# Kernel optimization log

Measured on AMD Instinct MI355X. Metric: run time of the kernel, lower is better.

Reference implementation:

```python
import jax, jax.numpy as jnp
import numpy as np

D_MODEL = 1024
NUM_HEADS = 16
D_HEAD = D_MODEL // NUM_HEADS
ROPE_THETA = 10000.0


def _rope(x, pos):
    # x: [..., S, d_head]; rotate consecutive pairs (2i, 2i+1)
    half = x.shape[-1] // 2
    inv_freq = ROPE_THETA ** (-jnp.arange(half, dtype=jnp.float32) * 2.0 / x.shape[-1])
    ang = pos[:, None].astype(jnp.float32) * inv_freq[None, :]  # [S, half]
    cos, sin = jnp.cos(ang), jnp.sin(ang)
    x1, x2 = x[..., 0::2], x[..., 1::2]
    r1 = x1 * cos - x2 * sin
    r2 = x1 * sin + x2 * cos
    return jnp.stack([r1, r2], axis=-1).reshape(x.shape)


def setup_inputs() -> dict:
    key = jax.random.key(0)
    ks = jax.random.split(key, 5)
    s = 1.0 / np.sqrt(D_MODEL)
    return {
        "q_weight": jax.random.normal(ks[0], (D_MODEL, D_MODEL), jnp.float32) * s,
        "k_weight": jax.random.normal(ks[1], (D_MODEL, D_MODEL), jnp.float32) * s,
        "v_weight": jax.random.normal(ks[2], (D_MODEL, D_MODEL), jnp.float32) * s,
        "o_weight": jax.random.normal(ks[3], (D_MODEL, D_MODEL), jnp.float32) * s,
        "in_features": jax.random.normal(ks[4], (2, 2048, D_MODEL), jnp.float32),
    }


def reference(q_weight, k_weight, v_weight, o_weight, in_features):
    S = in_features.shape[-2]
    qw = q_weight.reshape(NUM_HEADS, D_HEAD, D_MODEL)
    kw = k_weight.reshape(NUM_HEADS, D_HEAD, D_MODEL)
    vw = v_weight.reshape(NUM_HEADS, D_HEAD, D_MODEL)
    # [B, H, S, d_head]
    q = jnp.einsum('bsj,nhj->bnsh', in_features, qw)
    k = jnp.einsum('bsj,nhj->bnsh', in_features, kw)
    v = jnp.einsum('bsj,nhj->bnsh', in_features, vw)
    pos = jnp.arange(S)
    q = _rope(q, pos)
    k = _rope(k, pos)
    scale = 1.0 / jnp.sqrt(jnp.asarray(D_HEAD, dtype=q.dtype))
    scores = jnp.einsum('bnqh,bnkh->bnqk', q, k) * scale  # [B,H,S,S]
    causal = jnp.tril(jnp.ones((S, S), dtype=bool))
    scores = jnp.where(causal, scores, jnp.asarray(-jnp.inf, dtype=scores.dtype))
    attn = jax.nn.softmax(scores, axis=-1)
    out = jnp.einsum('bnqk,bnkh->bnqh', attn, v)  # [B,H,S,d_head]
    out = jnp.swapaxes(out, -2, -3).reshape(*out.shape[:-3], S, D_MODEL)
    return jnp.einsum('ji,bki->bkj', o_weight, out)
```

## Files before the change

### kernel.cpp

```cpp
#include <hip/hip_runtime.h>
#include <math.h>

typedef __attribute__((ext_vector_type(8))) short bf16x8;
typedef __attribute__((ext_vector_type(4))) short bf16x4;
typedef __attribute__((ext_vector_type(4))) float f32x4;
typedef __attribute__((ext_vector_type(2))) unsigned int u32x2;

static constexpr int D_MODEL = 1024;
static constexpr int SEQ = 2048;
static constexpr int BATCH = 2;
static constexpr int M_TOT = BATCH * SEQ;

__device__ __forceinline__ unsigned short f2bf(float f) {
  unsigned int u = __builtin_bit_cast(unsigned int, f);
  u += 0x7fffu + ((u >> 16) & 1u);
  return (unsigned short)(u >> 16);
}

__device__ __forceinline__ float bf2f(unsigned short u) {
  return __builtin_bit_cast(float, (unsigned int)u << 16);
}

__device__ __forceinline__ unsigned int cvtpk(float lo, float hi) {
  unsigned int r;
  asm volatile("v_cvt_pk_bf16_f32 %0, %1, %2" : "=v"(r) : "v"(lo), "v"(hi));
  return r;
}

__device__ __forceinline__ void gld16(const unsigned short* g, unsigned short* l) {
  __builtin_amdgcn_global_load_lds(
      (const __attribute__((address_space(1))) unsigned int*)g,
      (__attribute__((address_space(3))) unsigned int*)l, 16, 0, 0);
}

__global__ void prep_all(const float* __restrict__ x,
                         const float* __restrict__ qw, const float* __restrict__ kw,
                         const float* __restrict__ vw, const float* __restrict__ ow,
                         unsigned short* __restrict__ Xb,
                         unsigned short* __restrict__ Wqb,
                         float2* __restrict__ ct2) {
  constexpr int NX = M_TOT * D_MODEL / 4;
  constexpr int NW = D_MODEL * D_MODEL;
  const int i = blockIdx.x * blockDim.x + threadIdx.x;
  if (i < NX) {
    const float4 v = reinterpret_cast<const float4*>(x)[i];
    ushort4 o;
    o.x = f2bf(v.x); o.y = f2bf(v.y); o.z = f2bf(v.z); o.w = f2bf(v.w);
    reinterpret_cast<ushort4*>(Xb)[i] = o;
  } else if (i < NX + NW) {
    const int k = i - NX;
    const int which = k >> 18;
    const int off = k & 262143;
    const float* src = (which == 0) ? qw : (which == 1) ? kw : (which == 2) ? vw : ow;
    const float4 v = reinterpret_cast<const float4*>(src)[off];
    ushort4 o;
    o.x = f2bf(v.x); o.y = f2bf(v.y); o.z = f2bf(v.z); o.w = f2bf(v.w);
    reinterpret_cast<ushort4*>(Wqb)[k] = o;
  } else {
    const int k = i - NX - NW;
    const int s = k >> 5;
    const int p = k & 31;
    const float inv_freq = powf(10000.0f, -(float)p / 32.0f);
    const float ang = (float)s * inv_freq;
    const int psw = p ^ (((s >> 2) & 1) << 3);
    float2 cs; cs.x = cosf(ang); cs.y = sinf(ang);
    ct2[s * 32 + psw] = cs;
  }
}

template <int BM, int BN, int MODE>
__global__ __launch_bounds__(256, 2)
void gemm2(const unsigned short* __restrict__ A,
           const unsigned short* __restrict__ W,
           unsigned short* __restrict__ Qd,
           unsigned short* __restrict__ Kd,
           unsigned short* __restrict__ Vd,
           float* __restrict__ Fd,
           const float2* __restrict__ ct2) {
  constexpr int MI = BM / 32, NI = BN / 32;
  constexpr int NKT = D_MODEL / 64;
  constexpr int LOADS = BM / 32 + BN / 32;
  __shared__ __align__(16) unsigned short smem[2 * (BM + BN) * 64];
  unsigned short* Asm = smem;
  unsigned short* Bsm = smem + 2 * BM * 64;
  const int tid  = threadIdx.x;
  const int lane = tid & 63;
  const int wave = tid >> 6;
  const int wm = wave >> 1, wn = wave & 1;
  const int m0 = blockIdx.y * BM;
  const int n0 = blockIdx.x * BN;
  const int lr = lane & 15, lg = lane >> 4;

  auto stage = [&](int buf, int kt) {
    const int k0 = kt * 64;
#pragma unroll
    for (int c = 0; c < BM / 32; ++c) {
      const int ch = c * 4 + wave;
      const int row = ch * 8 + (lane >> 3);
      gld16(&A[(size_t)(m0 + row) * D_MODEL + k0 + ((lane & 7) ^ (row & 7)) * 8],
            &Asm[buf * BM * 64 + ch * 512]);
    }
#pragma unroll
    for (int c = 0; c < BN / 32; ++c) {
      const int ch = c * 4 + wave;
      const int row = ch * 8 + (lane >> 3);
      gld16(&W[(size_t)(n0 + row) * D_MODEL + k0 + ((lane & 7) ^ (row & 7)) * 8],
            &Bsm[buf * BN * 64 + ch * 512]);
    }
  };

  f32x4 acc[MI][NI] = {};

  stage(0, 0);
  stage(1, 1);
  __builtin_amdgcn_sched_barrier(0);

  for (int kt = 0; kt < NKT; ++kt) {
    const int cur = kt & 1;
    if (kt + 1 < NKT) {
      if constexpr (LOADS == 8) asm volatile("s_waitcnt vmcnt(8)" ::: "memory");
      else                      asm volatile("s_waitcnt vmcnt(6)" ::: "memory");
    } else {
      asm volatile("s_waitcnt vmcnt(0)" ::: "memory");
    }
    __builtin_amdgcn_s_barrier();
    __builtin_amdgcn_sched_barrier(0);

    bf16x8 af[MI][2], bfr[NI][2];
#pragma unroll
    for (int i = 0; i < MI; ++i)
#pragma unroll
      for (int ks = 0; ks < 2; ++ks) {
        const int R = wm * (BM / 2) + i * 16 + lr;
        const int p = (ks * 4 + lg) ^ (R & 7);
        af[i][ks] = *reinterpret_cast<const bf16x8*>(&Asm[cur * BM * 64 + R * 64 + p * 8]);
      }
#pragma unroll
    for (int j = 0; j < NI; ++j)
#pragma unroll
      for (int ks = 0; ks < 2; ++ks) {
        const int R = wn * (BN / 2) + j * 16 + lr;
        const int p = (ks * 4 + lg) ^ (R & 7);
        bfr[j][ks] = *reinterpret_cast<const bf16x8*>(&Bsm[cur * BN * 64 + R * 64 + p * 8]);
      }
    asm volatile("s_waitcnt lgkmcnt(0)" ::: "memory");
    __builtin_amdgcn_sched_barrier(0);
    __builtin_amdgcn_s_barrier();
    __builtin_amdgcn_sched_barrier(0);

    if (kt + 2 < NKT) stage(cur, kt + 2);
    __builtin_amdgcn_sched_barrier(0);

#pragma unroll
    for (int ks = 0; ks < 2; ++ks)
#pragma unroll
      for (int i = 0; i < MI; ++i)
#pragma unroll
        for (int j = 0; j < NI; ++j)
          acc[i][j] = __builtin_amdgcn_mfma_f32_16x16x32_bf16(af[i][ks], bfr[j][ks], acc[i][j], 0, 0, 0);
  }

  if constexpr (MODE == 2) {
#pragma unroll
    for (int i = 0; i < MI; ++i)
#pragma unroll
      for (int j = 0; j < NI; ++j)
#pragma unroll
        for (int r = 0; r < 4; ++r) {
          const int gm = m0 + wm * (BM / 2) + i * 16 + lg * 4 + r;
          const int gc = n0 + wn * (BN / 2) + j * 16 + lr;
          Fd[(size_t)gm * D_MODEL + gc] = acc[i][j][r];
        }
  } else {
    const int t = n0 >> 10;
    const int b = m0 >> 11;
    const int s_base = m0 & 2047;
    if (t < 2) {
      unsigned short* dstQ = (t == 0) ? Qd : Kd;
      const unsigned short* gsrc = (const unsigned short*)(ct2 + (size_t)s_base * 32);
#pragma unroll
      for (int it = 0; it < 8; ++it) {
        const int ch = wave * 8 + it;
        gld16(&gsrc[ch * 512 + lane * 8], &smem[ch * 512]);
      }
      asm volatile("s_waitcnt vmcnt(0)" ::: "memory");
      __builtin_amdgcn_sched_barrier(0);
      __builtin_amdgcn_s_barrier();
      const float2* tbl = (const float2*)smem;
      const int nbase = (n0 & 1023) >> 6;
#pragma unroll
      for (int i = 0; i < MI; ++i) {
#pragma unroll
        for (int j = 0; j < NI; ++j) {
#pragma unroll
          for (int r = 0; r < 4; ++r) {
            const int sl = wm * (BM / 2) + i * 16 + lg * 4 + r;
            const int h  = j * 16 + lr;
            const int psw = (h >> 1) ^ (((sl >> 2) & 1) << 3);
            const float2 cs = tbl[sl * 32 + psw];
            float x = acc[i][j][r];
            const float part = __shfl_xor(x, 1, 64);
            x = (h & 1) ? (part * cs.y + x * cs.x) : (x * cs.x - part * cs.y);
            const int n = nbase + wn;
            dstQ[(size_t)((b * 16 + n) * SEQ + s_base + sl) * 64 + h] = f2bf(x);
          }
        }
      }
    } else {
      unsigned short* tile = smem;
      const int row = tid >> 2;
      const int ck  = tid & 3;
      for (int pass = 0; pass < 2; ++pass) {
        __builtin_amdgcn_s_barrier();
        if (wn == pass) {
#pragma unroll
          for (int i = 0; i < MI; ++i)
#pragma unroll
            for (int j = 0; j < NI; ++j)
#pragma unroll
              for (int r = 0; r < 4; ++r)
                tile[(j * 16 + lr) * 136 + wm * 64 + i * 16 + lg * 4 + r] = f2bf(acc[i][j][r]);
        }
        asm volatile("s_waitcnt lgkmcnt(0)" ::: "memory");
        __builtin_amdgcn_sched_barrier(0);
        __builtin_amdgcn_s_barrier();
        const int c = (n0 & 1023) + pass * 64 + row;
        const int n = c >> 6, h = c & 63;
        unsigned short* vrow = &Vd[(size_t)((b * 16 + n) * 64 + h) * SEQ + s_base + ck * 32];
        const unsigned short* lrow = &tile[row * 136 + ck * 32];
#pragma unroll
        for (int k = 0; k < 4; ++k)
          *reinterpret_cast<bf16x8*>(&vrow[k * 8]) = *reinterpret_cast<const bf16x8*>(&lrow[k * 8]);
      }
    }
  }
}

__global__ __launch_bounds__(256, 2)
void attn_kernel(const unsigned short* __restrict__ Q,
                 const unsigned short* __restrict__ K,
                 const unsigned short* __restrict__ Vt,
                 unsigned short* __restrict__ AO,
                 unsigned short* __restrict__ po,
                 float* __restrict__ pl) {
  __shared__ __align__(16) unsigned short Ksh[2][4096];
  __shared__ __align__(16) unsigned short Vsh[2][4096];
  const int bn   = blockIdx.x;
  const int y    = blockIdx.y;
  const bool split = (y < 16);
  const int j    = split ? (15 - (y >> 1)) : (23 - y);
  const int half = split ? (y & 1) : 0;
  const int t0   = (split && half) ? (j + 1) : 0;
  const int tend = (split && !half) ? (j + 1) : (2 * j + 2);
  const int wave = threadIdx.x >> 6;
  const int lane = threadIdx.x & 63;
  const int lr = lane & 15, lg = lane >> 4;
  const int q0 = j * 128 + wave * 32;
  const unsigned short* Qh = Q  + (size_t)bn * SEQ * 64;
  const unsigned short* Kh = K  + (size_t)bn * SEQ * 64;
  const unsigned short* Vh = Vt + (size_t)bn * 64 * SEQ;
  const int b = bn >> 4, n = bn & 15;

  const int srow8 = lane >> 3;
  const int scolb = ((lane & 7) ^ srow8) * 8;

  auto stage = [&](int buf, int k0) {
#pragma unroll
    for (int c = 0; c < 2; ++c) {
      const int ch = wave * 2 + c;
      const int row = ch * 8 + srow8;
      gld16(&Kh[(size_t)(k0 + row) * 64 + scolb], &Ksh[buf][ch * 512]);
      gld16(&Vh[(size_t)row * SEQ + k0 + scolb], &Vsh[buf][ch * 512]);
    }
  };

  constexpr float KL2E = 0.125f * 1.44269504088896f;

  bf16x8 qf[2][2];
#pragma unroll
  for (int mi = 0; mi < 2; ++mi)
#pragma unroll
    for (int ks = 0; ks < 2; ++ks)
      qf[mi][ks] = *reinterpret_cast<const bf16x8*>(
          &Qh[(size_t)(q0 + mi * 16 + lr) * 64 + ks * 32 + lg * 8]);
  asm volatile("s_waitcnt vmcnt(0)" ::: "memory");
  __builtin_amdgcn_sched_barrier(0);

  f32x4 o[2][4] = {};
  float ls[2] = {0.f, 0.f};

  stage(0, t0 * 64);
  stage(1, (t0 + 1) * 64);
  __builtin_amdgcn_sched_barrier(0);

  for (int t = t0; t < tend; ++t) {
    const int cur = (t - t0) & 1;
    const int k0 = t * 64;
    if (t + 1 < tend) { asm volatile("s_waitcnt vmcnt(4)" ::: "memory"); }
    else              { asm volatile("s_waitcnt vmcnt(0)" ::: "memory"); }
    __builtin_amdgcn_s_barrier();
    __builtin_amdgcn_sched_barrier(0);

    const unsigned short* Kc = &Ksh[cur][0];
    const unsigned short* Vc = &Vsh[cur][0];

    bf16x8 kf[4][2];
#pragma unroll
    for (int nj = 0; nj < 4; ++nj)
#pragma unroll
      for (int ks = 0; ks < 2; ++ks) {
        const int R = nj * 16 + lr;
        const int p = (ks * 4 + lg) ^ (R & 7);
        kf[nj][ks] = *reinterpret_cast<const bf16x8*>(&Kc[R * 64 + p * 8]);
      }
    f32x4 sf[2][4] = {};
    __builtin_amdgcn_s_setprio(1);
#pragma unroll
    for (int nj = 0; nj < 4; ++nj)
#pragma unroll
      for (int ks = 0; ks < 2; ++ks)
#pragma unroll
        for (int mi = 0; mi < 2; ++mi)
          sf[mi][nj] = __builtin_amdgcn_mfma_f32_16x16x32_bf16(kf[nj][ks], qf[mi][ks], sf[mi][nj], 0, 0, 0);
    __builtin_amdgcn_s_setprio(0);

    bf16x4 vB[4][4];
#pragma unroll
    for (int nj = 0; nj < 4; ++nj)
#pragma unroll
      for (int hf = 0; hf < 4; ++hf) {
        const int R = hf * 16 + lr;
        const int c = nj * 2 + (lg >> 1);
        const int p = ((c ^ (R & 7)) << 3) + (lg & 1) * 4;
        vB[nj][hf] = *reinterpret_cast<const bf16x4*>(&Vc[R * 64 + p]);
      }

    u32x2 w[2][4];
    if (k0 + 63 <= q0) {
#pragma unroll
      for (int mi = 0; mi < 2; ++mi)
#pragma unroll
        for (int nj = 0; nj < 4; ++nj) {
          const float p0 = __builtin_amdgcn_exp2f(sf[mi][nj][0] * KL2E);
          const float p1 = __builtin_amdgcn_exp2f(sf[mi][nj][1] * KL2E);
          const float p2 = __builtin_amdgcn_exp2f(sf[mi][nj][2] * KL2E);
          const float p3 = __builtin_amdgcn_exp2f(sf[mi][nj][3] * KL2E);
          ls[mi] += (p0 + p1) + (p2 + p3);
          w[mi][nj][0] = cvtpk(p0, p1);
          w[mi][nj][1] = cvtpk(p2, p3);
        }
    } else {
#pragma unroll
      for (int mi = 0; mi < 2; ++mi) {
        const int qrow = q0 + mi * 16 + lr;
#pragma unroll
        for (int nj = 0; nj < 4; ++nj) {
          const int kb = k0 + nj * 16 + lg * 4;
          float p[4];
#pragma unroll
          for (int r = 0; r < 4; ++r)
            p[r] = (kb + r <= qrow) ? __builtin_amdgcn_exp2f(sf[mi][nj][r] * KL2E) : 0.0f;
          ls[mi] += (p[0] + p[1]) + (p[2] + p[3]);
          w[mi][nj][0] = cvtpk(p[0], p[1]);
          w[mi][nj][1] = cvtpk(p[2], p[3]);
        }
      }
    }

    asm volatile("s_waitcnt lgkmcnt(0)" ::: "memory");
    __builtin_amdgcn_sched_barrier(0);
    __builtin_amdgcn_s_barrier();
    __builtin_amdgcn_sched_barrier(0);

    if (t + 2 < tend) stage(cur, (t + 2) * 64);
    __builtin_amdgcn_sched_barrier(0);

    __builtin_amdgcn_s_setprio(1);
#pragma unroll
    for (int nj = 0; nj < 4; ++nj)
#pragma unroll
      for (int hf = 0; hf < 4; ++hf)
#pragma unroll
        for (int mi = 0; mi < 2; ++mi)
          o[mi][hf] = __builtin_amdgcn_mfma_f32_16x16x16bf16_1k(
              __builtin_bit_cast(bf16x4, w[mi][nj]), vB[nj][hf], o[mi][hf], 0, 0, 0);
    __builtin_amdgcn_s_setprio(0);
  }

#pragma unroll
  for (int mi = 0; mi < 2; ++mi) {
    float s = ls[mi];
    s += __shfl_xor(s, 16, 64);
    s += __shfl_xor(s, 32, 64);
    ls[mi] = s;
  }

  if (!split) {
#pragma unroll
    for (int mi = 0; mi < 2; ++mi)
#pragma unroll
      for (int r = 0; r < 4; ++r) {
        const float sv = __shfl(ls[mi], lg * 4 + r, 64);
        const float inv = 1.0f / sv;
        const int srow = q0 + mi * 16 + lg * 4 + r;
#pragma unroll
        for (int hf = 0; hf < 4; ++hf) {
          const int h = hf * 16 + lr;
          AO[(size_t)(b * SEQ + srow) * D_MODEL + n * 64 + h] = f2bf(o[mi][hf][r] * inv);
        }
      }
  } else {
    const int pb = (bn * 8 + (j - 8)) * 2 + half;
    unsigned short* pod = po + (size_t)pb * (128 * 64);
    float* pld = pl + (size_t)pb * 128;
    if (lg == 0) {
#pragma unroll
      for (int mi = 0; mi < 2; ++mi)
        pld[wave * 32 + mi * 16 + lr] = ls[mi];
    }
#pragma unroll
    for (int mi = 0; mi < 2; ++mi)
#pragma unroll
      for (int r = 0; r < 4; ++r) {
        const int row = wave * 32 + mi * 16 + lg * 4 + r;
#pragma unroll
        for (int hf = 0; hf < 4; ++hf)
          pod[row * 64 + hf * 16 + lr] = f2bf(o[mi][hf][r]);
      }
  }
}

__global__ void attn_merge(const unsigned short* __restrict__ po,
                           const float* __restrict__ pl,
                           unsigned short* __restrict__ AO) {
  const int i = blockIdx.x * blockDim.x + threadIdx.x;
  const int g   = i & 7;
  const int row = (i >> 3) & 127;
  const int jj  = (i >> 10) & 7;
  const int bn  = i >> 13;
  const int pb0 = (bn * 8 + jj) * 2;
  const float l = pl[pb0 * 128 + row] + pl[(pb0 + 1) * 128 + row];
  const float inv = 1.0f / l;
  const bf16x8 a = *reinterpret_cast<const bf16x8*>(&po[(size_t)pb0 * 8192 + row * 64 + g * 8]);
  const bf16x8 c = *reinterpret_cast<const bf16x8*>(&po[(size_t)(pb0 + 1) * 8192 + row * 64 + g * 8]);
  bf16x8 out;
#pragma unroll
  for (int e = 0; e < 8; ++e)
    out[e] = (short)f2bf((bf2f((unsigned short)a[e]) + bf2f((unsigned short)c[e])) * inv);
  const int s = (jj + 8) * 128 + row;
  const int b = bn >> 4, n = bn & 15;
  *reinterpret_cast<bf16x8*>(&AO[(size_t)(b * SEQ + s) * D_MODEL + n * 64 + g * 8]) = out;
}

extern "C" void kernel_launch(void* const* d_in, const int* in_sizes, int n_in,
                              void* d_out, int out_size, void* d_ws, size_t ws_size,
                              hipStream_t stream) {
  const float* qw = (const float*)d_in[0];
  const float* kw = (const float*)d_in[1];
  const float* vw = (const float*)d_in[2];
  const float* ow = (const float*)d_in[3];
  const float* x  = (const float*)d_in[4];

  char* ws = (char*)d_ws;
  const size_t XB = (size_t)M_TOT * D_MODEL * 2;
  const size_t WB = (size_t)D_MODEL * D_MODEL * 2;
  unsigned short* Xb  = (unsigned short*)ws;  ws += XB;
  unsigned short* Wqb = (unsigned short*)ws;  ws += WB;
  unsigned short* Wkb = (unsigned short*)ws;  ws += WB;
  unsigned short* Wvb = (unsigned short*)ws;  ws += WB;
  unsigned short* Wob = (unsigned short*)ws;  ws += WB;
  unsigned short* Qr  = (unsigned short*)ws;  ws += XB;
  unsigned short* Kr  = (unsigned short*)ws;  ws += XB;
  unsigned short* Vt  = (unsigned short*)ws;  ws += XB;
  unsigned short* AO  = (unsigned short*)ws;  ws += XB;
  float2* ct2 = (float2*)ws;  ws += (size_t)SEQ * 32 * 8;
  (void)Wkb; (void)Wvb;

  unsigned short* po = Xb;
  float*          pl = (float*)Wqb;

  constexpr int PREP_ITEMS = M_TOT * D_MODEL / 4 + D_MODEL * D_MODEL + SEQ * 32;
  prep_all<<<(PREP_ITEMS + 255) / 256, 256, 0, stream>>>(x, qw, kw, vw, ow, Xb, Wqb, ct2);

  gemm2<128, 128, 0><<<dim3(3072 / 128, M_TOT / 128), 256, 0, stream>>>(
      Xb, Wqb, Qr, Kr, Vt, nullptr, ct2);

  attn_kernel<<<dim3(BATCH * 16, 24), 256, 0, stream>>>(Qr, Kr, Vt, AO, po, pl);

  attn_merge<<<262144 / 256, 256, 0, stream>>>(po, pl, AO);

  gemm2<128, 64, 2><<<dim3(D_MODEL / 64, M_TOT / 128), 256, 0, stream>>>(
      AO, Wob, nullptr, nullptr, nullptr, (float*)d_out, nullptr);
}
```

Before: 102.8 us.

## Use two waves per attention block with 64 query rows each

The attention kernel now runs 2 waves of 64 query rows per block instead of 4 waves of 32 rows. Each K/V fragment read from shared memory therefore feeds twice as many MFMAs. The score, softmax and PV steps are restructured to loop per 16-row slice, which keeps the score registers small. The LDS barrier and next-tile prefetch now happen before compute rather than mid-loop. The trade-off is fewer waves per CU to hide latency, a larger output accumulator that raises register pressure, and each thread issuing twice as many loads during staging.

```diff
diff --git a/kernel.cpp b/kernel.cpp
--- a/kernel.cpp
+++ b/kernel.cpp
@@ -236,7 +236,7 @@
   }
 }
 
-__global__ __launch_bounds__(256, 2)
+__global__ __launch_bounds__(128, 2)
 void attn_kernel(const unsigned short* __restrict__ Q,
                  const unsigned short* __restrict__ K,
                  const unsigned short* __restrict__ Vt,
@@ -255,7 +255,7 @@
   const int wave = threadIdx.x >> 6;
   const int lane = threadIdx.x & 63;
   const int lr = lane & 15, lg = lane >> 4;
-  const int q0 = j * 128 + wave * 32;
+  const int q0 = j * 128 + wave * 64;
   const unsigned short* Qh = Q  + (size_t)bn * SEQ * 64;
   const unsigned short* Kh = K  + (size_t)bn * SEQ * 64;
   const unsigned short* Vh = Vt + (size_t)bn * 64 * SEQ;
@@ -266,8 +266,8 @@
 
   auto stage = [&](int buf, int k0) {
 #pragma unroll
-    for (int c = 0; c < 2; ++c) {
-      const int ch = wave * 2 + c;
+    for (int c = 0; c < 4; ++c) {
+      const int ch = wave * 4 + c;
       const int row = ch * 8 + srow8;
       gld16(&Kh[(size_t)(k0 + row) * 64 + scolb], &Ksh[buf][ch * 512]);
       gld16(&Vh[(size_t)row * SEQ + k0 + scolb], &Vsh[buf][ch * 512]);
@@ -276,9 +276,9 @@
 
   constexpr float KL2E = 0.125f * 1.44269504088896f;
 
-  bf16x8 qf[2][2];
-#pragma unroll
-  for (int mi = 0; mi < 2; ++mi)
+  bf16x8 qf[4][2];
+#pragma unroll
+  for (int mi = 0; mi < 4; ++mi)
 #pragma unroll
     for (int ks = 0; ks < 2; ++ks)
       qf[mi][ks] = *reinterpret_cast<const bf16x8*>(
@@ -286,8 +286,8 @@
   asm volatile("s_waitcnt vmcnt(0)" ::: "memory");
   __builtin_amdgcn_sched_barrier(0);
 
-  f32x4 o[2][4] = {};
-  float ls[2] = {0.f, 0.f};
+  f32x4 o[4][4] = {};
+  float ls[4] = {0.f, 0.f, 0.f, 0.f};
 
   stage(0, t0 * 64);
   stage(1, (t0 + 1) * 64);
@@ -296,7 +296,7 @@
   for (int t = t0; t < tend; ++t) {
     const int cur = (t - t0) & 1;
     const int k0 = t * 64;
-    if (t + 1 < tend) { asm volatile("s_waitcnt vmcnt(4)" ::: "memory"); }
+    if (t + 1 < tend) { asm volatile("s_waitcnt vmcnt(8)" ::: "memory"); }
     else              { asm volatile("s_waitcnt vmcnt(0)" ::: "memory"); }
     __builtin_amdgcn_s_barrier();
     __builtin_amdgcn_sched_barrier(0);
@@ -313,17 +313,6 @@
         const int p = (ks * 4 + lg) ^ (R & 7);
         kf[nj][ks] = *reinterpret_cast<const bf16x8*>(&Kc[R * 64 + p * 8]);
       }
-    f32x4 sf[2][4] = {};
-    __builtin_amdgcn_s_setprio(1);
-#pragma unroll
-    for (int nj = 0; nj < 4; ++nj)
-#pragma unroll
-      for (int ks = 0; ks < 2; ++ks)
-#pragma unroll
-        for (int mi = 0; mi < 2; ++mi)
-          sf[mi][nj] = __builtin_amdgcn_mfma_f32_16x16x32_bf16(kf[nj][ks], qf[mi][ks], sf[mi][nj], 0, 0, 0);
-    __builtin_amdgcn_s_setprio(0);
-
     bf16x4 vB[4][4];
 #pragma unroll
     for (int nj = 0; nj < 4; ++nj)
@@ -334,24 +323,40 @@
         const int p = ((c ^ (R & 7)) << 3) + (lg & 1) * 4;
         vB[nj][hf] = *reinterpret_cast<const bf16x4*>(&Vc[R * 64 + p]);
       }
-
-    u32x2 w[2][4];
-    if (k0 + 63 <= q0) {
-#pragma unroll
-      for (int mi = 0; mi < 2; ++mi)
+    asm volatile("s_waitcnt lgkmcnt(0)" ::: "memory");
+    __builtin_amdgcn_sched_barrier(0);
+    __builtin_amdgcn_s_barrier();
+    __builtin_amdgcn_sched_barrier(0);
+
+    if (t + 2 < tend) stage(cur, (t + 2) * 64);
+    __builtin_amdgcn_sched_barrier(0);
+
+    const bool full = (k0 + 63 <= q0);
+
+#pragma unroll
+    for (int mi = 0; mi < 4; ++mi) {
+      f32x4 sf[4] = {};
+      __builtin_amdgcn_s_setprio(1);
+#pragma unroll
+      for (int nj = 0; nj < 4; ++nj)
+#pragma unroll
+        for (int ks = 0; ks < 2; ++ks)
+          sf[nj] = __builtin_amdgcn_mfma_f32_16x16x32_bf16(kf[nj][ks], qf[mi][ks], sf[nj], 0, 0, 0);
+      __builtin_amdgcn_s_setprio(0);
+
+      u32x2 w[4];
+      if (full) {
 #pragma unroll
         for (int nj = 0; nj < 4; ++nj) {
-          const float p0 = __builtin_amdgcn_exp2f(sf[mi][nj][0] * KL2E);
-          const float p1 = __builtin_amdgcn_exp2f(sf[mi][nj][1] * KL2E);
-          const float p2 = __builtin_amdgcn_exp2f(sf[mi][nj][2] * KL2E);
-          const float p3 = __builtin_amdgcn_exp2f(sf[mi][nj][3] * KL2E);
+          const float p0 = __builtin_amdgcn_exp2f(sf[nj][0] * KL2E);
+          const float p1 = __builtin_amdgcn_exp2f(sf[nj][1] * KL2E);
+          const float p2 = __builtin_amdgcn_exp2f(sf[nj][2] * KL2E);
+          const float p3 = __builtin_amdgcn_exp2f(sf[nj][3] * KL2E);
           ls[mi] += (p0 + p1) + (p2 + p3);
-          w[mi][nj][0] = cvtpk(p0, p1);
-          w[mi][nj][1] = cvtpk(p2, p3);
-        }
-    } else {
-#pragma unroll
-      for (int mi = 0; mi < 2; ++mi) {
+          w[nj][0] = cvtpk(p0, p1);
+          w[nj][1] = cvtpk(p2, p3);
+        }
+      } else {
         const int qrow = q0 + mi * 16 + lr;
 #pragma unroll
         for (int nj = 0; nj < 4; ++nj) {
@@ -359,36 +364,26 @@
           float p[4];
 #pragma unroll
           for (int r = 0; r < 4; ++r)
-            p[r] = (kb + r <= qrow) ? __builtin_amdgcn_exp2f(sf[mi][nj][r] * KL2E) : 0.0f;
+            p[r] = (kb + r <= qrow) ? __builtin_amdgcn_exp2f(sf[nj][r] * KL2E) : 0.0f;
           ls[mi] += (p[0] + p[1]) + (p[2] + p[3]);
-          w[mi][nj][0] = cvtpk(p[0], p[1]);
-          w[mi][nj][1] = cvtpk(p[2], p[3]);
-        }
-      }
-    }
-
-    asm volatile("s_waitcnt lgkmcnt(0)" ::: "memory");
-    __builtin_amdgcn_sched_barrier(0);
-    __builtin_amdgcn_s_barrier();
-    __builtin_amdgcn_sched_barrier(0);
-
-    if (t + 2 < tend) stage(cur, (t + 2) * 64);
-    __builtin_amdgcn_sched_barrier(0);
-
-    __builtin_amdgcn_s_setprio(1);
-#pragma unroll
-    for (int nj = 0; nj < 4; ++nj)
-#pragma unroll
-      for (int hf = 0; hf < 4; ++hf)
-#pragma unroll
-        for (int mi = 0; mi < 2; ++mi)
+          w[nj][0] = cvtpk(p[0], p[1]);
+          w[nj][1] = cvtpk(p[2], p[3]);
+        }
+      }
+
+      __builtin_amdgcn_s_setprio(1);
+#pragma unroll
+      for (int nj = 0; nj < 4; ++nj)
+#pragma unroll
+        for (int hf = 0; hf < 4; ++hf)
           o[mi][hf] = __builtin_amdgcn_mfma_f32_16x16x16bf16_1k(
-              __builtin_bit_cast(bf16x4, w[mi][nj]), vB[nj][hf], o[mi][hf], 0, 0, 0);
-    __builtin_amdgcn_s_setprio(0);
-  }
-
-#pragma unroll
-  for (int mi = 0; mi < 2; ++mi) {
+              __builtin_bit_cast(bf16x4, w[nj]), vB[nj][hf], o[mi][hf], 0, 0, 0);
+      __builtin_amdgcn_s_setprio(0);
+    }
+  }
+
+#pragma unroll
+  for (int mi = 0; mi < 4; ++mi) {
     float s = ls[mi];
     s += __shfl_xor(s, 16, 64);
     s += __shfl_xor(s, 32, 64);
@@ -397,7 +392,7 @@
 
   if (!split) {
 #pragma unroll
-    for (int mi = 0; mi < 2; ++mi)
+    for (int mi = 0; mi < 4; ++mi)
 #pragma unroll
       for (int r = 0; r < 4; ++r) {
         const float sv = __shfl(ls[mi], lg * 4 + r, 64);
@@ -415,14 +410,14 @@
     float* pld = pl + (size_t)pb * 128;
     if (lg == 0) {
 #pragma unroll
-      for (int mi = 0; mi < 2; ++mi)
-        pld[wave * 32 + mi * 16 + lr] = ls[mi];
-    }
-#pragma unroll
-    for (int mi = 0; mi < 2; ++mi)
+      for (int mi = 0; mi < 4; ++mi)
+        pld[wave * 64 + mi * 16 + lr] = ls[mi];
+    }
+#pragma unroll
+    for (int mi = 0; mi < 4; ++mi)
 #pragma unroll
       for (int r = 0; r < 4; ++r) {
-        const int row = wave * 32 + mi * 16 + lg * 4 + r;
+        const int row = wave * 64 + mi * 16 + lg * 4 + r;
 #pragma unroll
         for (int hf = 0; hf < 4; ++hf)
           pod[row * 64 + hf * 16 + lr] = f2bf(o[mi][hf][r]);
@@ -485,7 +480,7 @@
   gemm2<128, 128, 0><<<dim3(3072 / 128, M_TOT / 128), 256, 0, stream>>>(
       Xb, Wqb, Qr, Kr, Vt, nullptr, ct2);
 
-  attn_kernel<<<dim3(BATCH * 16, 24), 256, 0, stream>>>(Qr, Kr, Vt, AO, po, pl);
+  attn_kernel<<<dim3(BATCH * 16, 24), 128, 0, stream>>>(Qr, Kr, Vt, AO, po, pl);
 
   attn_merge<<<262144 / 256, 256, 0, stream>>>(po, pl, AO);
 
```

New measurement: 113.9 us. 1.11x slower.
